# Kernel optimization log

Hardware: AMD Instinct MI355X
Metric: run time of the kernel (lower is better)

Reference implementation:

```python
import jax, jax.numpy as jnp
from jax import lax
import numpy as np

B, L, CIN, H, OUT = 512, 1024, 6, 64, 1  # N(time-for-LSTM), L(lstm batch), input_dim, hidden_dim, output_dim
EPS = 1e-5


def setup_inputs() -> dict:
    key = jax.random.key(0)
    ks = jax.random.split(key, 20)
    rn = lambda k, s, sc=0.1: jax.random.normal(k, s, jnp.float32) * sc
    return {
        "inputs": rn(ks[0], (B, L, CIN), 1.0),
        "hidden_state": jnp.zeros((1, L, H), jnp.float32),
        "cell_state": jnp.zeros((1, L, H), jnp.float32),
        "conv1_w": rn(ks[1], (H, CIN, 2)), "conv1_b": rn(ks[2], (H,)),
        "bn1_gamma": jnp.ones((H,), jnp.float32), "bn1_beta": jnp.zeros((H,), jnp.float32),
        "bn1_mean": rn(ks[3], (H,)), "bn1_var": jax.random.uniform(ks[4], (H,), jnp.float32, 0.5, 1.5),
        "conv2_w": rn(ks[5], (H, H, 2)), "conv2_b": rn(ks[6], (H,)),
        "bn2_gamma": jnp.ones((H,), jnp.float32), "bn2_beta": jnp.zeros((H,), jnp.float32),
        "bn2_mean": rn(ks[7], (H,)), "bn2_var": jax.random.uniform(ks[8], (H,), jnp.float32, 0.5, 1.5),
        "tc1_w": rn(ks[9], (H, H, 2)), "tc1_b": rn(ks[10], (H,)),  # ConvTranspose1d weight: (Cin, Cout, K)
        "bn3_gamma": jnp.ones((H,), jnp.float32), "bn3_beta": jnp.zeros((H,), jnp.float32),
        "bn3_mean": rn(ks[11], (H,)), "bn3_var": jax.random.uniform(ks[12], (H,), jnp.float32, 0.5, 1.5),
        "tc2_w": rn(ks[13], (H, H, 2)), "tc2_b": rn(ks[14], (H,)),
        "w_ih": rn(ks[15], (4 * H, H)), "w_hh": rn(ks[16], (4 * H, H)),
        "b_ih": rn(ks[17], (4 * H,)), "b_hh": rn(ks[18], (4 * H,)),
        "out_w": rn(ks[19], (OUT, H)), "out_b": jnp.zeros((OUT,), jnp.float32),
    }


def _bn(x, g, b, m, v):  # eval-mode BatchNorm1d on (N, C, L)
    scale = g / jnp.sqrt(v + EPS)
    return (x - m[None, :, None]) * scale[None, :, None] + b[None, :, None]


def _conv(x, w, b):  # valid Conv1d, w: (Cout, Cin, K)
    y = lax.conv_general_dilated(x, w, (1,), 'VALID', dimension_numbers=('NCH', 'OIH', 'NCH'))
    return y + b[None, :, None]


def _convT(x, w, b):  # stride-1 ConvTranspose1d == full corr with flipped kernel; w: (Cin, Cout, K)
    k = w.shape[2]
    wk = jnp.transpose(jnp.flip(w, axis=2), (1, 0, 2))  # (Cout, Cin, K)
    y = lax.conv_general_dilated(x, wk, (1,), [(k - 1, k - 1)], dimension_numbers=('NCH', 'OIH', 'NCH'))
    return y + b[None, :, None]


def _lstm(x, h0, c0, w_ih, w_hh, b_ih, b_hh):  # x: (T, Lb, H); torch gate order i,f,g,o
    bias = b_ih + b_hh
    def step(carry, xt):
        h, c = carry
        z = xt @ w_ih.T + h @ w_hh.T + bias
        i, f, g, o = jnp.split(z, 4, axis=-1)
        c = jax.nn.sigmoid(f) * c + jax.nn.sigmoid(i) * jnp.tanh(g)
        h = jax.nn.sigmoid(o) * jnp.tanh(c)
        return (h, c), h
    (hT, cT), ys = lax.scan(step, (h0, c0), x)
    return ys, hT, cT


def _forward(inputs, hidden_state, cell_state, conv1_w, conv1_b, bn1_gamma, bn1_beta, bn1_mean, bn1_var,
             conv2_w, conv2_b, bn2_gamma, bn2_beta, bn2_mean, bn2_var,
             tc1_w, tc1_b, bn3_gamma, bn3_beta, bn3_mean, bn3_var,
             tc2_w, tc2_b, w_ih, w_hh, b_ih, b_hh, out_w, out_b):
    x = jnp.transpose(inputs, (0, 2, 1))                                     # (N, Cin, L)
    x = jax.nn.relu(_bn(_conv(x, conv1_w, conv1_b), bn1_gamma, bn1_beta, bn1_mean, bn1_var))  # (N,H,L-1)
    x = jax.nn.relu(_bn(_conv(x, conv2_w, conv2_b), bn2_gamma, bn2_beta, bn2_mean, bn2_var))  # (N,H,L-2)
    x = jax.nn.relu(_bn(_convT(x, tc1_w, tc1_b), bn3_gamma, bn3_beta, bn3_mean, bn3_var))     # (N,H,L-1)
    x = jax.nn.relu(_convT(x, tc2_w, tc2_b))                                  # (N,H,L)
    x = jnp.transpose(x, (0, 2, 1))                                           # (N, L, H): time=N, batch=L
    ys, hT, cT = _lstm(x, hidden_state[0], cell_state[0], w_ih, w_hh, b_ih, b_hh)
    outputs = ys @ out_w.T + out_b                                            # (N, L, OUT)
    return outputs, hT[None], cT[None]


def reference(inputs, hidden_state, cell_state, conv1_w, conv1_b, bn1_gamma, bn1_beta, bn1_mean, bn1_var,
              conv2_w, conv2_b, bn2_gamma, bn2_beta, bn2_mean, bn2_var,
              tc1_w, tc1_b, bn3_gamma, bn3_beta, bn3_mean, bn3_var,
              tc2_w, tc2_b, w_ih, w_hh, b_ih, b_hh, out_w, out_b):
    return _forward(inputs, hidden_state, cell_state, conv1_w, conv1_b, bn1_gamma, bn1_beta, bn1_mean, bn1_var,
                    conv2_w, conv2_b, bn2_gamma, bn2_beta, bn2_mean, bn2_var,
                    tc1_w, tc1_b, bn3_gamma, bn3_beta, bn3_mean, bn3_var,
                    tc2_w, tc2_b, w_ih, w_hh, b_ih, b_hh, out_w, out_b)
```

## Files before the change

### kernel.cpp

```cpp
#include <hip/hip_runtime.h>
#include <hip/hip_bf16.h>
#include <stdint.h>


typedef __attribute__((ext_vector_type(8))) short bf16x8;
typedef __attribute__((ext_vector_type(4))) float f32x4;

__device__ __forceinline__ uint16_t f2bf(float f) {
  union { float f; uint32_t i; } v; v.f = f;
  return (uint16_t)((v.i + 0x7FFFu + ((v.i >> 16) & 1u)) >> 16);
}
__device__ __forceinline__ float frcp(float x) { return __builtin_amdgcn_rcpf(x); }
__device__ __forceinline__ float fsig2(float z)  { return frcp(1.f + __builtin_amdgcn_exp2f(-z)); }
__device__ __forceinline__ float ftanh2(float z) { return 1.f - 2.f * frcp(1.f + __builtin_amdgcn_exp2f(z)); }

#define MFMA16(a, b, c) __builtin_amdgcn_mfma_f32_16x16x32_bf16(a, b, c, 0, 0, 0)

__global__ __launch_bounds__(256) void prep_k(
    const float* __restrict__ w2p, const float* __restrict__ t1p,
    const float* __restrict__ t2p,
    const float* __restrict__ g1, const float* __restrict__ be1,
    const float* __restrict__ m1, const float* __restrict__ v1,
    const float* __restrict__ b1,
    const float* __restrict__ g2, const float* __restrict__ be2,
    const float* __restrict__ m2, const float* __restrict__ v2,
    const float* __restrict__ b2,
    const float* __restrict__ g3, const float* __restrict__ be3,
    const float* __restrict__ m3, const float* __restrict__ v3,
    const float* __restrict__ tb1, const float* __restrict__ tb2,
    uint16_t* __restrict__ W)
{
  int idx = blockIdx.x * 256 + threadIdx.x;
  if (idx < 8192) {
    int h = idx >> 7, k = idx & 127;
    W[idx] = f2bf(w2p[h * 128 + (k & 63) * 2 + (k >> 6)]);
  } else if (idx < 16384) {
    int i = idx - 8192; int h = i >> 7, k = i & 127;
    W[idx] = f2bf(t1p[(k & 63) * 128 + h * 2 + (k >> 6)]);
  } else if (idx < 24576) {
    int i = idx - 16384; int h = i >> 7, k = i & 127;
    W[idx] = f2bf(t2p[(k & 63) * 128 + h * 2 + (k >> 6)]);
  } else if (idx < 25088) {
    int i = idx - 24576;
    float* F = (float*)(W + 24576);
    int h = i & 63, sel = i >> 6;
    float val;
    if (sel == 0)      val = g1[h] * __builtin_amdgcn_rsqf(v1[h] + 1e-5f);
    else if (sel == 1) { float s = g1[h] * __builtin_amdgcn_rsqf(v1[h] + 1e-5f);
                         val = (b1[h] - m1[h]) * s + be1[h]; }
    else if (sel == 2) val = g2[h] * __builtin_amdgcn_rsqf(v2[h] + 1e-5f);
    else if (sel == 3) { float s = g2[h] * __builtin_amdgcn_rsqf(v2[h] + 1e-5f);
                         val = (b2[h] - m2[h]) * s + be2[h]; }
    else if (sel == 4) val = g3[h] * __builtin_amdgcn_rsqf(v3[h] + 1e-5f);
    else if (sel == 5) { float s = g3[h] * __builtin_amdgcn_rsqf(v3[h] + 1e-5f);
                         val = (tb1[h] - m3[h]) * s + be3[h]; }
    else if (sel == 6) val = 1.0f;
    else               val = tb2[h];
    F[i] = val;
  }
}

#define YT   72
#define NROW 84

template<int PHASE>
__device__ __forceinline__ void mfma_phase(
    const uint16_t* yin, uint16_t* yout, uint16_t* Xg,
    const uint16_t* __restrict__ wAg,
    const float* __restrict__ p_sc, const float* __restrict__ p_tc,
    int lane, int wv, int l0)
{
  const int m0 = wv * 16;
  const int lm = lane & 15, lq = lane >> 4;
  bf16x8 af[4];
#pragma unroll
  for (int kc = 0; kc < 4; ++kc)
    af[kc] = *(const bf16x8*)&wAg[(m0 + lm) * 128 + kc * 32 + lq * 8];
  float scr[4], tcr[4];
#pragma unroll
  for (int r = 0; r < 4; ++r) {
    int hr = m0 + lq * 4 + r;
    scr[r] = p_sc[hr]; tcr[r] = p_tc[hr];
  }
  const f32x4 Z = {0.f, 0.f, 0.f, 0.f};
#pragma unroll
  for (int nt = 0; nt < 5; ++nt) {
    f32x4 acc = Z;
#pragma unroll
    for (int kc = 0; kc < 4; ++kc) {
      int half = kc >> 1;
      int rT = nt * 16 + lm + 1 + (PHASE == 2 ? half : -half);
      bf16x8 bf_ = *(const bf16x8*)&yin[rT * YT + (kc & 1) * 32 + lq * 8];
      acc = MFMA16(af[kc], bf_, acc);
    }
    int il = nt * 16 + lm;
    int gl = l0 - 2 + il;
#pragma unroll
    for (int r = 0; r < 4; ++r) {
      int h = m0 + lq * 4 + r;
      float v = fmaxf(acc[r] * scr[r] + tcr[r], 0.f);
      if constexpr (PHASE == 2) {
        if (il < 66) yout[(il + 1) * YT + h] = (gl >= 0 && gl < 1022) ? f2bf(v) : (uint16_t)0;
      } else if constexpr (PHASE == 3) {
        if (il >= 1 && il < 66) yout[(il + 1) * YT + h] = (gl >= 0 && gl < 1023) ? f2bf(v) : (uint16_t)0;
      } else {
        if (il >= 2 && il < 66) Xg[(size_t)gl * 64 + h] = f2bf(v);
      }
    }
  }
}

__global__ __launch_bounds__(256, 6) void conv_stack_k(
    const float* __restrict__ inp, const float* __restrict__ w1p,
    const float* __restrict__ F,
    const uint16_t* __restrict__ W2a, const uint16_t* __restrict__ T1a,
    const uint16_t* __restrict__ T2a,
    uint16_t* __restrict__ X)
{
  __shared__ __align__(16) uint16_t yTA[NROW * YT];
  __shared__ __align__(16) uint16_t yTB[NROW * YT];
  __shared__ float xs[6][YT];
  const int tid  = threadIdx.x;
  const int lane = tid & 63;
  const int wv   = tid >> 6;
  const int t    = blockIdx.y;
  const int l0   = blockIdx.x * 64;

  for (int i = tid; i < 6 * YT; i += 256) {
    int c = i % 6, il = i / 6;
    int gl = l0 - 2 + il;
    float v = 0.f;
    if (gl >= 0 && gl < 1024) v = inp[(size_t)t * 6144 + (size_t)gl * 6 + c];
    xs[c][il] = v;
  }

  {
    const int h = lane;
    float wr[12];
#pragma unroll
    for (int i = 0; i < 6; ++i) {
      float2 q = *(const float2*)(w1p + h * 12 + i * 2);
      wr[i * 2] = q.x; wr[i * 2 + 1] = q.y;
    }
    float sc = F[h], tc = F[64 + h];
    __syncthreads();
#pragma unroll 1
    for (int base = wv * 4; base < 67; base += 16) {
      float a0 = 0, a1 = 0, a2 = 0, a3 = 0;
#pragma unroll
      for (int c = 0; c < 6; ++c) {
        float4 v = *(const float4*)&xs[c][base];
        float s4 = xs[c][base + 4];
        float k0 = wr[c * 2], k1 = wr[c * 2 + 1];
        a0 += v.x * k0 + v.y * k1;
        a1 += v.y * k0 + v.z * k1;
        a2 += v.z * k0 + v.w * k1;
        a3 += v.w * k0 + s4 * k1;
      }
      float r[4] = {a0, a1, a2, a3};
#pragma unroll
      for (int j = 0; j < 4; ++j) {
        int il = base + j;
        if (il < 67) {
          int gl = l0 - 2 + il;
          yTA[(il + 1) * YT + h] =
              (gl >= 0 && gl < 1023) ? f2bf(fmaxf(r[j] * sc + tc, 0.f)) : (uint16_t)0;
        }
      }
    }
  }
  __syncthreads();

  mfma_phase<2>(yTA, yTB, nullptr, W2a, F + 128, F + 192, lane, wv, l0);
  __syncthreads();
  mfma_phase<3>(yTB, yTA, nullptr, T1a, F + 256, F + 320, lane, wv, l0);
  __syncthreads();
  mfma_phase<4>(yTA, nullptr, X + (size_t)(t + 1) * 65536, T2a,
                F + 384, F + 448, lane, wv, l0);
}

#define HSTR 72

#define LSTM_STEP(T_, K_, AXC, DG, XD, AXN) do {                               \
    bf16x8 hf0_ = *(const bf16x8*)&hh[((K_) + 7) & 7][(lm >> 2) * HSTR + lq * 8];      \
    bf16x8 hf1_ = *(const bf16x8*)&hh[((K_) + 7) & 7][(lm >> 2) * HSTR + 32 + lq * 8]; \
    if ((((K_) & 3) == 0) && (T_) > 0 && wv == (((T_) >> 2) & 3)) {            \
      bf16x8 pa0_ = *(const bf16x8*)&hh[((K_) ^ 4) + (lm & 3)][(lm >> 2) * HSTR + lq * 8];      \
      bf16x8 pa1_ = *(const bf16x8*)&hh[((K_) ^ 4) + (lm & 3)][(lm >> 2) * HSTR + 32 + lq * 8]; \
      f32x4 pr_ = MFMA16(pa1_, owf1, MFMA16(pa0_, owf0, Z4));                  \
      if (lm == 0) {                                                           \
        outp[(size_t)((T_) - 4) * 1024 + l0 + lq] = pr_[0] + obv;              \
        outp[(size_t)((T_) - 3) * 1024 + l0 + lq] = pr_[1] + obv;              \
        outp[(size_t)((T_) - 2) * 1024 + l0 + lq] = pr_[2] + obv;              \
        outp[(size_t)((T_) - 1) * 1024 + l0 + lq] = pr_[3] + obv;              \
      }                                                                        \
    }                                                                          \
    f32x4 z0_ = MFMA16(hf1_, bfr[0][3], MFMA16(hf0_, bfr[0][2], AXC[0]));      \
    f32x4 z1_ = MFMA16(hf1_, bfr[1][3], MFMA16(hf0_, bfr[1][2], AXC[1]));      \
    f32x4 z2_ = MFMA16(hf1_, bfr[2][3], MFMA16(hf0_, bfr[2][2], AXC[2]));      \
    f32x4 z3_ = MFMA16(hf1_, bfr[3][3], MFMA16(hf0_, bfr[3][2], AXC[3]));      \
    float ii_ = fsig2(z0_[(K_) & 3]);                                          \
    float ff_ = fsig2(z1_[(K_) & 3]);                                          \
    float gg_ = ftanh2(z2_[(K_) & 3]);                                         \
    float oo_ = fsig2(z3_[(K_) & 3]);                                          \
    creg  = ff_ * creg + ii_ * gg_;                                            \
    float th_ = 1.f - 2.f * frcp(1.f + __builtin_amdgcn_exp2f(creg * 2.88539008177793f)); \
    hprev = oo_ * th_;                                                         \
    uint32_t hw_;                                                              \
    asm("v_cvt_pk_bf16_f32 %0, %1, %2" : "=v"(hw_) : "v"(hprev), "v"(0.f));    \
    hh[(K_)][lq * HSTR + hcol] = (uint16_t)hw_;                                \
    AXN[DG] = MFMA16(XD[1], bfr[DG][1], MFMA16(XD[0], bfr[DG][0], seeds[DG])); \
    asm volatile("s_waitcnt lgkmcnt(0)" ::: "memory");                         \
    __builtin_amdgcn_s_barrier();                                              \
    asm volatile("" ::: "memory");                                             \
  } while (0)

__global__ __launch_bounds__(256) void lstm_k(
    const float* __restrict__ h0p, const float* __restrict__ c0p,
    const float* __restrict__ wihp, const float* __restrict__ whhp,
    const float* __restrict__ bihp, const float* __restrict__ bhhp,
    const float* __restrict__ owp, const float* __restrict__ obp,
    uint16_t* __restrict__ Xb, float* __restrict__ outp)
{
  __shared__ __align__(16) uint16_t hh[8][4 * HSTR];
  const int tid  = threadIdx.x;
  const int lane = tid & 63;
  const int wv   = tid >> 6;
  const int lm   = lane & 15;
  const int lq   = lane >> 4;
  const int l0   = blockIdx.x << 2;
  const int hcol = (wv << 4) | lm;
  const f32x4 Z4 = {0.f, 0.f, 0.f, 0.f};
  const float L2E = 1.44269504088896340736f;

  bf16x8 bfr[4][4];
#pragma unroll
  for (int nt = 0; nt < 4; ++nt) {
    float sg = (nt == 2) ? 2.f * L2E : L2E;
    int n = nt * 64 + hcol;
#pragma unroll
    for (int kc = 0; kc < 4; ++kc) {
      int k0 = kc * 32 + lq * 8;
      const float* src = (k0 < 64) ? (wihp + (size_t)n * 64 + k0)
                                   : (whhp + (size_t)n * 64 + (k0 - 64));
      bf16x8 f;
#pragma unroll
      for (int j = 0; j < 8; ++j) f[j] = (short)f2bf(src[j] * sg);
      bfr[nt][kc] = f;
    }
  }
  float bi0 = (bihp[hcol]       + bhhp[hcol])       * L2E;
  float bi1 = (bihp[64 + hcol]  + bhhp[64 + hcol])  * L2E;
  float bi2 = (bihp[128 + hcol] + bhhp[128 + hcol]) * 2.f * L2E;
  float bi3 = (bihp[192 + hcol] + bhhp[192 + hcol]) * L2E;
  f32x4 seeds[4];
  seeds[0] = f32x4{bi0, bi0, bi0, bi0};
  seeds[1] = f32x4{bi1, bi1, bi1, bi1};
  seeds[2] = f32x4{bi2, bi2, bi2, bi2};
  seeds[3] = f32x4{bi3, bi3, bi3, bi3};
  float obv = obp[0];

  bf16x8 owf0 = {0, 0, 0, 0, 0, 0, 0, 0}, owf1 = {0, 0, 0, 0, 0, 0, 0, 0};
  if (lm == 0) {
#pragma unroll
    for (int j = 0; j < 8; ++j) {
      owf0[j] = (short)f2bf(owp[lq * 8 + j]);
      owf1[j] = (short)f2bf(owp[32 + lq * 8 + j]);
    }
  }

  float creg  = c0p[(size_t)(l0 + lq) * 64 + hcol];
  float hprev = 0.f;

  {
    int row = tid >> 6, col = tid & 63;
    hh[7][row * HSTR + col] = f2bf(h0p[(size_t)(l0 + row) * 64 + col]);
  }

  const uint16_t* pA = Xb + (size_t)(1 + (lm & 3)) * 65536
                     + (size_t)(l0 + (lm >> 2)) * 64 + lq * 8;
  const uint16_t* pB = pA + (size_t)4 * 65536;
  bf16x8 xA[2], xB[2];
  xA[0] = *(const bf16x8*)pA; xA[1] = *(const bf16x8*)(pA + 32);
  pA += (size_t)8 * 65536;
  xB[0] = *(const bf16x8*)pB; xB[1] = *(const bf16x8*)(pB + 32);
  pB += (size_t)8 * 65536;

  f32x4 axA[4], axB[4];
#pragma unroll
  for (int g = 0; g < 4; ++g)
    axA[g] = MFMA16(xA[1], bfr[g][1], MFMA16(xA[0], bfr[g][0], seeds[g]));
  __syncthreads();

#pragma unroll 1
  for (int t0 = 0; t0 < 512; t0 += 8) {
    if (t0 + 8 < 512) {
      xA[0] = *(const bf16x8*)pA; xA[1] = *(const bf16x8*)(pA + 32);
      pA += (size_t)8 * 65536;
    }
    LSTM_STEP(t0 + 0, 0, axA, 0, xB, axB);
    LSTM_STEP(t0 + 1, 1, axA, 1, xB, axB);
    LSTM_STEP(t0 + 2, 2, axA, 2, xB, axB);
    LSTM_STEP(t0 + 3, 3, axA, 3, xB, axB);
    if (t0 + 12 < 512) {
      xB[0] = *(const bf16x8*)pB; xB[1] = *(const bf16x8*)(pB + 32);
      pB += (size_t)8 * 65536;
    }
    LSTM_STEP(t0 + 4, 4, axB, 0, xA, axA);
    LSTM_STEP(t0 + 5, 5, axB, 1, xA, axA);
    LSTM_STEP(t0 + 6, 6, axB, 2, xA, axA);
    LSTM_STEP(t0 + 7, 7, axB, 3, xA, axA);
  }

  if (wv == 0) {
    bf16x8 pa0 = *(const bf16x8*)&hh[4 + (lm & 3)][(lm >> 2) * HSTR + lq * 8];
    bf16x8 pa1 = *(const bf16x8*)&hh[4 + (lm & 3)][(lm >> 2) * HSTR + 32 + lq * 8];
    f32x4 pr = MFMA16(pa1, owf1, MFMA16(pa0, owf0, Z4));
    if (lm == 0) {
      outp[(size_t)508 * 1024 + l0 + lq] = pr[0] + obv;
      outp[(size_t)509 * 1024 + l0 + lq] = pr[1] + obv;
      outp[(size_t)510 * 1024 + l0 + lq] = pr[2] + obv;
      outp[(size_t)511 * 1024 + l0 + lq] = pr[3] + obv;
    }
  }

  outp[524288 + (size_t)(l0 + lq) * 64 + hcol] = hprev;
  outp[589824 + (size_t)(l0 + lq) * 64 + hcol] = creg;
}

extern "C" void kernel_launch(void* const* d_in, const int* in_sizes, int n_in,
                              void* d_out, int out_size, void* d_ws, size_t ws_size,
                              hipStream_t stream)
{
  (void)in_sizes; (void)n_in; (void)out_size;
  if (ws_size < (size_t)513 * 65536 * 2) return;

  const float* inp = (const float*)d_in[0];
  const float* h0p = (const float*)d_in[1];
  const float* c0p = (const float*)d_in[2];
  const float* w1  = (const float*)d_in[3];
  const float* b1  = (const float*)d_in[4];
  const float* g1  = (const float*)d_in[5];
  const float* be1 = (const float*)d_in[6];
  const float* m1  = (const float*)d_in[7];
  const float* v1  = (const float*)d_in[8];
  const float* w2  = (const float*)d_in[9];
  const float* b2  = (const float*)d_in[10];
  const float* g2  = (const float*)d_in[11];
  const float* be2 = (const float*)d_in[12];
  const float* m2  = (const float*)d_in[13];
  const float* v2  = (const float*)d_in[14];
  const float* tw1 = (const float*)d_in[15];
  const float* tb1 = (const float*)d_in[16];
  const float* g3  = (const float*)d_in[17];
  const float* be3 = (const float*)d_in[18];
  const float* m3  = (const float*)d_in[19];
  const float* v3  = (const float*)d_in[20];
  const float* tw2 = (const float*)d_in[21];
  const float* tb2 = (const float*)d_in[22];
  const float* wih = (const float*)d_in[23];
  const float* whh = (const float*)d_in[24];
  const float* bih = (const float*)d_in[25];
  const float* bhh = (const float*)d_in[26];
  const float* ow  = (const float*)d_in[27];
  const float* ob  = (const float*)d_in[28];

  uint16_t* Xb   = (uint16_t*)d_ws;
  float*    outp = (float*)d_out;

  const uint16_t* W2a = Xb;
  const uint16_t* T1a = Xb + 8192;
  const uint16_t* T2a = Xb + 16384;
  const float*    F   = (const float*)(Xb + 24576);

  prep_k<<<98, 256, 0, stream>>>(w2, tw1, tw2,
                                 g1, be1, m1, v1, b1,
                                 g2, be2, m2, v2, b2,
                                 g3, be3, m3, v3, tb1, tb2, Xb);
  conv_stack_k<<<dim3(16, 512), 256, 0, stream>>>(inp, w1, F, W2a, T1a, T2a, Xb);
  lstm_k<<<256, 256, 0, stream>>>(h0p, c0p, wih, whh, bih, bhh, ow, ob, Xb, outp);
}
```

Before: 220.5 us.

## Offload LSTM output projection to a dedicated fifth wavefront

Adds a fifth wave to each LSTM block that only computes the output projection from the shared hidden-state ring buffer. It joins the per-step barriers so it stays in lockstep with the four recurrence waves. This takes the occasional projection MFMA and global stores off the critical recurrent path, which previously ran on one of the compute waves every fourth step. The cost is an extra wave per block and more waves at each barrier, and correctness depends on the barrier counts matching exactly.

```diff
diff --git a/kernel.cpp b/kernel.cpp
--- a/kernel.cpp
+++ b/kernel.cpp
@@ -181,20 +181,15 @@
 
 #define HSTR 72
 
+#define BARRIER() do {                                                         \
+    asm volatile("s_waitcnt lgkmcnt(0)" ::: "memory");                         \
+    __builtin_amdgcn_s_barrier();                                              \
+    asm volatile("" ::: "memory");                                             \
+  } while (0)
+
 #define LSTM_STEP(T_, K_, AXC, DG, XD, AXN) do {                               \
     bf16x8 hf0_ = *(const bf16x8*)&hh[((K_) + 7) & 7][(lm >> 2) * HSTR + lq * 8];      \
     bf16x8 hf1_ = *(const bf16x8*)&hh[((K_) + 7) & 7][(lm >> 2) * HSTR + 32 + lq * 8]; \
-    if ((((K_) & 3) == 0) && (T_) > 0 && wv == (((T_) >> 2) & 3)) {            \
-      bf16x8 pa0_ = *(const bf16x8*)&hh[((K_) ^ 4) + (lm & 3)][(lm >> 2) * HSTR + lq * 8];      \
-      bf16x8 pa1_ = *(const bf16x8*)&hh[((K_) ^ 4) + (lm & 3)][(lm >> 2) * HSTR + 32 + lq * 8]; \
-      f32x4 pr_ = MFMA16(pa1_, owf1, MFMA16(pa0_, owf0, Z4));                  \
-      if (lm == 0) {                                                           \
-        outp[(size_t)((T_) - 4) * 1024 + l0 + lq] = pr_[0] + obv;              \
-        outp[(size_t)((T_) - 3) * 1024 + l0 + lq] = pr_[1] + obv;              \
-        outp[(size_t)((T_) - 2) * 1024 + l0 + lq] = pr_[2] + obv;              \
-        outp[(size_t)((T_) - 1) * 1024 + l0 + lq] = pr_[3] + obv;              \
-      }                                                                        \
-    }                                                                          \
     f32x4 z0_ = MFMA16(hf1_, bfr[0][3], MFMA16(hf0_, bfr[0][2], AXC[0]));      \
     f32x4 z1_ = MFMA16(hf1_, bfr[1][3], MFMA16(hf0_, bfr[1][2], AXC[1]));      \
     f32x4 z2_ = MFMA16(hf1_, bfr[2][3], MFMA16(hf0_, bfr[2][2], AXC[2]));      \
@@ -210,12 +205,10 @@
     asm("v_cvt_pk_bf16_f32 %0, %1, %2" : "=v"(hw_) : "v"(hprev), "v"(0.f));    \
     hh[(K_)][lq * HSTR + hcol] = (uint16_t)hw_;                                \
     AXN[DG] = MFMA16(XD[1], bfr[DG][1], MFMA16(XD[0], bfr[DG][0], seeds[DG])); \
-    asm volatile("s_waitcnt lgkmcnt(0)" ::: "memory");                         \
-    __builtin_amdgcn_s_barrier();                                              \
-    asm volatile("" ::: "memory");                                             \
+    BARRIER();                                                                 \
   } while (0)
 
-__global__ __launch_bounds__(256) void lstm_k(
+__global__ __launch_bounds__(320) void lstm_k(
     const float* __restrict__ h0p, const float* __restrict__ c0p,
     const float* __restrict__ wihp, const float* __restrict__ whhp,
     const float* __restrict__ bihp, const float* __restrict__ bhhp,
@@ -229,8 +222,66 @@
   const int lm   = lane & 15;
   const int lq   = lane >> 4;
   const int l0   = blockIdx.x << 2;
+  const f32x4 Z4 = {0.f, 0.f, 0.f, 0.f};
+
+  if (tid < 256) {
+    int row = tid >> 6, col = tid & 63;
+    hh[7][row * HSTR + col] = f2bf(h0p[(size_t)(l0 + row) * 64 + col]);
+  }
+  __syncthreads();
+
+  if (wv == 4) {
+    bf16x8 owf0 = {0, 0, 0, 0, 0, 0, 0, 0}, owf1 = {0, 0, 0, 0, 0, 0, 0, 0};
+    if (lm == 0) {
+#pragma unroll
+      for (int j = 0; j < 8; ++j) {
+        owf0[j] = (short)f2bf(owp[lq * 8 + j]);
+        owf1[j] = (short)f2bf(owp[32 + lq * 8 + j]);
+      }
+    }
+    float obv = obp[0];
+#pragma unroll 1
+    for (int t0 = 0; t0 < 512; t0 += 8) {
+      if (t0 > 0) {
+        bf16x8 pa0 = *(const bf16x8*)&hh[4 + (lm & 3)][(lm >> 2) * HSTR + lq * 8];
+        bf16x8 pa1 = *(const bf16x8*)&hh[4 + (lm & 3)][(lm >> 2) * HSTR + 32 + lq * 8];
+        f32x4 pr = MFMA16(pa1, owf1, MFMA16(pa0, owf0, Z4));
+        if (lm == 0) {
+          outp[(size_t)(t0 - 4) * 1024 + l0 + lq] = pr[0] + obv;
+          outp[(size_t)(t0 - 3) * 1024 + l0 + lq] = pr[1] + obv;
+          outp[(size_t)(t0 - 2) * 1024 + l0 + lq] = pr[2] + obv;
+          outp[(size_t)(t0 - 1) * 1024 + l0 + lq] = pr[3] + obv;
+        }
+      }
+      BARRIER(); BARRIER(); BARRIER(); BARRIER();
+      {
+        bf16x8 pa0 = *(const bf16x8*)&hh[(lm & 3)][(lm >> 2) * HSTR + lq * 8];
+        bf16x8 pa1 = *(const bf16x8*)&hh[(lm & 3)][(lm >> 2) * HSTR + 32 + lq * 8];
+        f32x4 pr = MFMA16(pa1, owf1, MFMA16(pa0, owf0, Z4));
+        if (lm == 0) {
+          outp[(size_t)(t0 + 0) * 1024 + l0 + lq] = pr[0] + obv;
+          outp[(size_t)(t0 + 1) * 1024 + l0 + lq] = pr[1] + obv;
+          outp[(size_t)(t0 + 2) * 1024 + l0 + lq] = pr[2] + obv;
+          outp[(size_t)(t0 + 3) * 1024 + l0 + lq] = pr[3] + obv;
+        }
+      }
+      BARRIER(); BARRIER(); BARRIER(); BARRIER();
+    }
+    {
+      bf16x8 pa0 = *(const bf16x8*)&hh[4 + (lm & 3)][(lm >> 2) * HSTR + lq * 8];
+      bf16x8 pa1 = *(const bf16x8*)&hh[4 + (lm & 3)][(lm >> 2) * HSTR + 32 + lq * 8];
+      f32x4 pr = MFMA16(pa1, owf1, MFMA16(pa0, owf0, Z4));
+      if (lm == 0) {
+        outp[(size_t)508 * 1024 + l0 + lq] = pr[0] + obv;
+        outp[(size_t)509 * 1024 + l0 + lq] = pr[1] + obv;
+        outp[(size_t)510 * 1024 + l0 + lq] = pr[2] + obv;
+        outp[(size_t)511 * 1024 + l0 + lq] = pr[3] + obv;
+      }
+    }
+    return;
+  }
+
   const int hcol = (wv << 4) | lm;
-  const f32x4 Z4 = {0.f, 0.f, 0.f, 0.f};
   const float L2E = 1.44269504088896340736f;
 
   bf16x8 bfr[4][4];
@@ -258,24 +309,9 @@
   seeds[1] = f32x4{bi1, bi1, bi1, bi1};
   seeds[2] = f32x4{bi2, bi2, bi2, bi2};
   seeds[3] = f32x4{bi3, bi3, bi3, bi3};
-  float obv = obp[0];
-
-  bf16x8 owf0 = {0, 0, 0, 0, 0, 0, 0, 0}, owf1 = {0, 0, 0, 0, 0, 0, 0, 0};
-  if (lm == 0) {
-#pragma unroll
-    for (int j = 0; j < 8; ++j) {
-      owf0[j] = (short)f2bf(owp[lq * 8 + j]);
-      owf1[j] = (short)f2bf(owp[32 + lq * 8 + j]);
-    }
-  }
 
   float creg  = c0p[(size_t)(l0 + lq) * 64 + hcol];
   float hprev = 0.f;
-
-  {
-    int row = tid >> 6, col = tid & 63;
-    hh[7][row * HSTR + col] = f2bf(h0p[(size_t)(l0 + row) * 64 + col]);
-  }
 
   const uint16_t* pA = Xb + (size_t)(1 + (lm & 3)) * 65536
                      + (size_t)(l0 + (lm >> 2)) * 64 + lq * 8;
@@ -290,7 +326,6 @@
 #pragma unroll
   for (int g = 0; g < 4; ++g)
     axA[g] = MFMA16(xA[1], bfr[g][1], MFMA16(xA[0], bfr[g][0], seeds[g]));
-  __syncthreads();
 
 #pragma unroll 1
   for (int t0 = 0; t0 < 512; t0 += 8) {
@@ -310,18 +345,6 @@
     LSTM_STEP(t0 + 5, 5, axB, 1, xA, axA);
     LSTM_STEP(t0 + 6, 6, axB, 2, xA, axA);
     LSTM_STEP(t0 + 7, 7, axB, 3, xA, axA);
-  }
-
-  if (wv == 0) {
-    bf16x8 pa0 = *(const bf16x8*)&hh[4 + (lm & 3)][(lm >> 2) * HSTR + lq * 8];
-    bf16x8 pa1 = *(const bf16x8*)&hh[4 + (lm & 3)][(lm >> 2) * HSTR + 32 + lq * 8];
-    f32x4 pr = MFMA16(pa1, owf1, MFMA16(pa0, owf0, Z4));
-    if (lm == 0) {
-      outp[(size_t)508 * 1024 + l0 + lq] = pr[0] + obv;
-      outp[(size_t)509 * 1024 + l0 + lq] = pr[1] + obv;
-      outp[(size_t)510 * 1024 + l0 + lq] = pr[2] + obv;
-      outp[(size_t)511 * 1024 + l0 + lq] = pr[3] + obv;
-    }
   }
 
   outp[524288 + (size_t)(l0 + lq) * 64 + hcol] = hprev;
@@ -378,5 +401,5 @@
                                  g2, be2, m2, v2, b2,
                                  g3, be3, m3, v3, tb1, tb2, Xb);
   conv_stack_k<<<dim3(16, 512), 256, 0, stream>>>(inp, w1, F, W2a, T1a, T2a, Xb);
-  lstm_k<<<256, 256, 0, stream>>>(h0p, c0p, wih, whh, bih, bhh, ow, ob, Xb, outp);
-}
+  lstm_k<<<256, 320, 0, stream>>>(h0p, c0p, wih, whh, bih, bhh, ow, ob, Xb, outp);
+}
```

Result: faster. 209.2 us (-5.2%).
